# Performance work log

Hardware: AMD Instinct MI355X
Metric: run time of the kernel (lower is better)

## Reference

```python
import jax, jax.numpy as jnp
import numpy as np

BETA_MAX = 0.01
CD_WEIGHT = 1.0
FIDELITY_WEIGHT = 0.5
BETA = BETA_MAX  # fully annealed (step >= beta_warmup)
EPS = 1e-12


def _pairwise_dist(a, b):
    """Euclidean distance matrix. a: [B,N,3], b: [B,M,3] -> [B,N,M]."""
    a2 = jnp.sum(a * a, axis=-1)                      # [B,N]
    b2 = jnp.sum(b * b, axis=-1)                      # [B,M]
    ab = jnp.einsum('bnd,bmd->bnm', a, b)             # [B,N,M]
    sq = a2[:, :, None] + b2[:, None, :] - 2.0 * ab
    return jnp.sqrt(jnp.maximum(sq, EPS))


def chamfer_distance_l1(pred, full):
    d = _pairwise_dist(pred, full)                    # [B,N,M]
    d_pf = jnp.min(d, axis=2)                         # pred -> full, [B,N]
    d_fp = jnp.min(d, axis=1)                         # full -> pred, [B,M]
    return 0.5 * (jnp.mean(d_pf) + jnp.mean(d_fp))


def fidelity_loss(partial, pred):
    # one-directional: every partial point should have a close predicted point
    d = _pairwise_dist(partial, pred)                 # [B,P,N]
    return jnp.mean(jnp.min(d, axis=2))


def kl_divergence(mu, logvar):
    # -0.5 * E_batch[ sum_dim (1 + logvar - mu^2 - exp(logvar)) ]
    kl = -0.5 * jnp.sum(1.0 + logvar - mu * mu - jnp.exp(logvar), axis=1)
    return jnp.mean(kl)


def setup_inputs() -> dict:
    key = jax.random.key(0)
    k1, k2, k3, k4, k5 = jax.random.split(key, 5)
    B, N, P, D = 8, 8192, 2048, 512
    return {
        'pred': jax.random.normal(k1, (B, N, 3), dtype=jnp.float32),
        'full': jax.random.normal(k2, (B, N, 3), dtype=jnp.float32),
        'partial': jax.random.normal(k3, (B, P, 3), dtype=jnp.float32),
        'mu': jax.random.normal(k4, (B, D), dtype=jnp.float32),
        'logvar': jax.random.normal(k5, (B, D), dtype=jnp.float32) * 0.1,
    }


def reference(pred, full, partial, mu, logvar):
    cd = chamfer_distance_l1(pred, full)
    kl = kl_divergence(mu, logvar)
    fidel = fidelity_loss(partial, pred)
    total = CD_WEIGHT * cd + BETA * kl + FIDELITY_WEIGHT * fidel
    return (total, cd, kl, fidel)
```

## Files before the change

kernel.cpp:

```cpp
#include <hip/hip_runtime.h>
#include <math.h>

#define BATCH 8
#define NPTS  8192
#define PPTS  2048
#define DLAT  512

typedef __attribute__((ext_vector_type(8)))  short short8;
typedef __attribute__((ext_vector_type(16))) float floatx16;

#define SEG      (2 * BATCH * NPTS + BATCH * PPTS)
#define DIR_PF   0
#define DIR_FP   (BATCH * NPTS)
#define DIR_FID  (2 * BATCH * NPTS)
#define OFF_SEG  8

#define CHUNK  512
#define XBLK   512

__device__ __forceinline__ unsigned short f2bf(float f) {
    unsigned int u = __float_as_uint(f);
    return (unsigned short)((u + 0x7FFFu + ((u >> 16) & 1u)) >> 16);
}
__device__ __forceinline__ float bf2f(unsigned short s) {
    return __uint_as_float(((unsigned int)s) << 16);
}

__device__ __forceinline__ float min16(floatx16 d, float prev) {
    float a0 = fminf(fminf(d[0],  d[1]),  d[2]);
    float a1 = fminf(fminf(d[3],  d[4]),  d[5]);
    float a2 = fminf(fminf(d[6],  d[7]),  d[8]);
    float a3 = fminf(fminf(d[9],  d[10]), d[11]);
    float a4 = fminf(fminf(d[12], d[13]), d[14]);
    float b0 = fminf(fminf(a0, a1), a2);
    float b1 = fminf(fminf(a3, a4), d[15]);
    return fminf(fminf(b0, b1), prev);
}

__device__ __forceinline__ void encodeY(float y0, float y1, float y2,
                                        uint4* r0, uint4* r1) {
    const unsigned short h0 = f2bf(y0), h1 = f2bf(y1), h2 = f2bf(y2);
    const unsigned short l0 = f2bf(y0 - bf2f(h0));
    const unsigned short l1 = f2bf(y1 - bf2f(h1));
    const unsigned short l2 = f2bf(y2 - bf2f(h2));
    const float yn = fmaf(y0, y0, fmaf(y1, y1, y2 * y2));
    const unsigned short nh = f2bf(yn);
    const unsigned short nl = f2bf(yn - bf2f(nh));
    r0->x = (unsigned int)h0 | ((unsigned int)h1 << 16);
    r0->y = (unsigned int)h2 | ((unsigned int)l0 << 16);
    r0->z = (unsigned int)l1 | ((unsigned int)l2 << 16);
    r0->w = (unsigned int)h0 | ((unsigned int)h1 << 16);
    r1->x = (unsigned int)h2 | ((unsigned int)nh << 16);
    r1->y = (unsigned int)nl;
    r1->z = 0u; r1->w = 0u;
}

__global__ __launch_bounds__(256, 4) void minpass_kernel(
        const float* __restrict__ pred,
        const float* __restrict__ full,
        const float* __restrict__ partial,
        float* __restrict__ wsf,
        int ysplit) {
    const int bid = blockIdx.x;
    const int ys  = bid % ysplit;
    const int r   = bid / ysplit;
    const int b   = r / 36;
    const int s   = r % 36;
    const int yhalf = NPTS / ysplit;

    const int t = threadIdx.x;

    if (bid == 0) {
        if (t < 4) wsf[t] = 0.0f;
        if (t == 4) ((unsigned int*)wsf)[4] = 0u;
    }

    const float* xset; const float* yset; int minoff; int xbase;
    if (s < 16)      { xset = pred;    yset = full; xbase = b*NPTS + s*XBLK;
                       minoff = OFF_SEG + ys*SEG + DIR_PF  + b*NPTS + s*XBLK; }
    else if (s < 32) { xset = full;    yset = pred; xbase = b*NPTS + (s-16)*XBLK;
                       minoff = OFF_SEG + ys*SEG + DIR_FP  + b*NPTS + (s-16)*XBLK; }
    else             { xset = partial; yset = pred; xbase = b*PPTS + (s-32)*XBLK;
                       minoff = OFF_SEG + ys*SEG + DIR_FID + b*PPTS + (s-32)*XBLK; }

    const int lane = t & 63;
    const int wid  = t >> 6;
    const int l31  = lane & 31;
    const int half = lane >> 5;

    __shared__ uint4 sY[2][CHUNK];
    __shared__ uint4 sX[2][XBLK];
    __shared__ float sXn[XBLK];

    for (int i = t; i < XBLK; i += 256) {
        const float* xp = xset + (size_t)(xbase + i) * 3;
        const float x0 = xp[0], x1 = xp[1], x2 = xp[2];
        const float m0 = -2.0f*x0, m1 = -2.0f*x1, m2 = -2.0f*x2;
        const unsigned short h0 = f2bf(m0), h1 = f2bf(m1), h2 = f2bf(m2);
        const unsigned short l0 = f2bf(m0 - bf2f(h0));
        const unsigned short l1 = f2bf(m1 - bf2f(h1));
        const unsigned short l2 = f2bf(m2 - bf2f(h2));
        const unsigned int one = 0x3F80u;
        uint4 r0, r1;
        r0.x = (unsigned int)h0 | ((unsigned int)h1 << 16);
        r0.y = (unsigned int)h2 | ((unsigned int)h0 << 16);
        r0.z = (unsigned int)h1 | ((unsigned int)h2 << 16);
        r0.w = (unsigned int)l0 | ((unsigned int)l1 << 16);
        r1.x = (unsigned int)l2 | (one << 16);
        r1.y = one;
        r1.z = 0u; r1.w = 0u;
        sX[0][i] = r0; sX[1][i] = r1;
        sXn[i] = fmaf(x0, x0, fmaf(x1, x1, x2 * x2));
    }
    __syncthreads();

    const int xw = wid * 128;
    const short8 bf0 = *(const short8*)&sX[half][xw + l31];
    const short8 bf1 = *(const short8*)&sX[half][xw + 32 + l31];
    const short8 bf2 = *(const short8*)&sX[half][xw + 64 + l31];
    const short8 bf3 = *(const short8*)&sX[half][xw + 96 + l31];
    const float  xn0 = sXn[xw + l31];
    const float  xn1 = sXn[xw + 32 + l31];
    const float  xn2 = sXn[xw + 64 + l31];
    const float  xn3 = sXn[xw + 96 + l31];

    const floatx16 zc = {0,0,0,0, 0,0,0,0, 0,0,0,0, 0,0,0,0};
    float cmin0 = 3.4e38f, cmin1 = 3.4e38f, cmin2 = 3.4e38f, cmin3 = 3.4e38f;

    const float* ypts = yset + (size_t)(b * NPTS + ys * yhalf) * 3;

    for (int c = 0; c < yhalf; c += CHUNK) {
        __syncthreads();
        for (int i = t; i < CHUNK; i += 256) {
            const float* yp = ypts + (size_t)(c + i) * 3;
            uint4 r0, r1;
            encodeY(yp[0], yp[1], yp[2], &r0, &r1);
            sY[0][i] = r0; sY[1][i] = r1;
        }
        __syncthreads();

        const uint4* sYh = &sY[half][0];
        short8 af = *(const short8*)&sYh[l31];
#pragma unroll
        for (int j = 0; j < CHUNK / 32; ++j) {
            short8 afn = af;
            if (j + 1 < CHUNK / 32)
                afn = *(const short8*)&sYh[(j + 1) * 32 + l31];
            const floatx16 d0 = __builtin_amdgcn_mfma_f32_32x32x16_bf16(af, bf0, zc, 0, 0, 0);
            const floatx16 d1 = __builtin_amdgcn_mfma_f32_32x32x16_bf16(af, bf1, zc, 0, 0, 0);
            cmin0 = min16(d0, cmin0);
            const floatx16 d2 = __builtin_amdgcn_mfma_f32_32x32x16_bf16(af, bf2, zc, 0, 0, 0);
            cmin1 = min16(d1, cmin1);
            const floatx16 d3 = __builtin_amdgcn_mfma_f32_32x32x16_bf16(af, bf3, zc, 0, 0, 0);
            cmin2 = min16(d2, cmin2);
            cmin3 = min16(d3, cmin3);
            af = afn;
        }
    }

    const float m0 = fminf(cmin0, __shfl_xor(cmin0, 32, 64));
    const float m1 = fminf(cmin1, __shfl_xor(cmin1, 32, 64));
    const float m2 = fminf(cmin2, __shfl_xor(cmin2, 32, 64));
    const float m3 = fminf(cmin3, __shfl_xor(cmin3, 32, 64));
    if (lane < 32) {
        wsf[minoff + xw + l31]      = fmaxf(m0 + xn0, 0.0f);
        wsf[minoff + xw + 32 + l31] = fmaxf(m1 + xn1, 0.0f);
        wsf[minoff + xw + 64 + l31] = fmaxf(m2 + xn2, 0.0f);
        wsf[minoff + xw + 96 + l31] = fmaxf(m3 + xn3, 0.0f);
    }
}

__device__ __forceinline__ float waveReduceSum(float v) {
#pragma unroll
    for (int o = 32; o > 0; o >>= 1) v += __shfl_down(v, o, 64);
    return v;
}

__device__ __forceinline__ float blockReduceSum(float v) {
    __shared__ float wsum[4];
    const int lane = threadIdx.x & 63;
    const int wid  = threadIdx.x >> 6;
    v = waveReduceSum(v);
    if (lane == 0) wsum[wid] = v;
    __syncthreads();
    if (wid == 0) {
        v = (lane < ((int)blockDim.x >> 6)) ? wsum[lane] : 0.0f;
        v = waveReduceSum(v);
    }
    return v;
}

#define NRED_BLOCKS 145
__global__ __launch_bounds__(256) void reduce_finalize_kernel(
        float* __restrict__ wsf,
        const float* __restrict__ mu,
        const float* __restrict__ logvar,
        float* __restrict__ out,
        int ysplit) {
    float* acc = wsf;
    unsigned int* cnt = (unsigned int*)wsf + 4;
    const int bid = blockIdx.x;
    const int t   = threadIdx.x;

    float v = 0.0f;
    int accIdx;
    if (bid < 144) {
        int base;
        if (bid < 64)       { accIdx = 0; base = DIR_PF  + bid * 1024;         }
        else if (bid < 128) { accIdx = 1; base = DIR_FP  + (bid - 64) * 1024;  }
        else                { accIdx = 2; base = DIR_FID + (bid - 128) * 1024; }
#pragma unroll
        for (int k = 0; k < 4; ++k) {
            const int i = OFF_SEG + base + k * 256 + t;
            float m = wsf[i];
            for (int sg = 1; sg < ysplit; ++sg) m = fminf(m, wsf[sg * SEG + i]);
            v += sqrtf(fmaxf(m, 1e-12f));
        }
    } else {
        accIdx = 3;
#pragma unroll
        for (int k = 0; k < BATCH * DLAT / 256; ++k) {
            const int i = k * 256 + t;
            const float m = mu[i];
            const float l = logvar[i];
            v += -0.5f * (1.0f + l - m * m - expf(l));
        }
    }

    v = blockReduceSum(v);
    if (t == 0) {
        atomicAdd(&acc[accIdx], v);
        __threadfence();
        const unsigned int done = atomicAdd(cnt, 1u);
        if (done == NRED_BLOCKS - 1) {
            const float s_pf  = atomicAdd(&acc[0], 0.0f);
            const float s_fp  = atomicAdd(&acc[1], 0.0f);
            const float s_fid = atomicAdd(&acc[2], 0.0f);
            const float s_kl  = atomicAdd(&acc[3], 0.0f);
            const float cd  = 0.5f * (s_pf / (float)(BATCH * NPTS) +
                                      s_fp / (float)(BATCH * NPTS));
            const float fid = s_fid / (float)(BATCH * PPTS);
            const float kl  = s_kl / (float)BATCH;
            out[0] = cd + 0.01f * kl + 0.5f * fid;
            out[1] = cd;
            out[2] = kl;
            out[3] = fid;
        }
    }
}

extern "C" void kernel_launch(void* const* d_in, const int* in_sizes, int n_in,
                              void* d_out, int out_size, void* d_ws, size_t ws_size,
                              hipStream_t stream) {
    const float* pred    = (const float*)d_in[0];
    const float* full    = (const float*)d_in[1];
    const float* partial = (const float*)d_in[2];
    const float* mu      = (const float*)d_in[3];
    const float* logvar  = (const float*)d_in[4];
    float* out = (float*)d_out;
    float* wsf = (float*)d_ws;

    const size_t need4 = (size_t)(OFF_SEG + 4 * SEG) * 4;
    const int ysplit = (ws_size >= need4) ? 4 : 2;

    minpass_kernel<<<8 * 36 * ysplit, 256, 0, stream>>>(pred, full, partial, wsf, ysplit);

    reduce_finalize_kernel<<<NRED_BLOCKS, 256, 0, stream>>>(wsf, mu, logvar, out, ysplit);
}
```

Measured before the change: 104.7 us.

## Use v_min3 for min reduction, load X operands directly, widen reduce grid

The 16-way min reduction now uses inline v_min3_f32 instructions instead of chained fminf calls. Each lane builds its MFMA B-operand fragments and norms straight from global memory, which removes the shared-memory staging of X and one block barrier. The finalize kernel goes from 145 to 577 blocks, each reducing 256 elements instead of 1024, to raise parallelism. In exchange, the atomic-add contention on the accumulators and the completion counter rises, and each X point is encoded redundantly by both half-waves.

```diff
diff --git a/kernel.cpp b/kernel.cpp
--- a/kernel.cpp
+++ b/kernel.cpp
@@ -26,15 +26,21 @@
     return __uint_as_float(((unsigned int)s) << 16);
 }
 
+__device__ __forceinline__ float min3f(float a, float b, float c) {
+    float d;
+    asm("v_min3_f32 %0, %1, %2, %3" : "=v"(d) : "v"(a), "v"(b), "v"(c));
+    return d;
+}
+
 __device__ __forceinline__ float min16(floatx16 d, float prev) {
-    float a0 = fminf(fminf(d[0],  d[1]),  d[2]);
-    float a1 = fminf(fminf(d[3],  d[4]),  d[5]);
-    float a2 = fminf(fminf(d[6],  d[7]),  d[8]);
-    float a3 = fminf(fminf(d[9],  d[10]), d[11]);
-    float a4 = fminf(fminf(d[12], d[13]), d[14]);
-    float b0 = fminf(fminf(a0, a1), a2);
-    float b1 = fminf(fminf(a3, a4), d[15]);
-    return fminf(fminf(b0, b1), prev);
+    const float a0 = min3f(d[0],  d[1],  d[2]);
+    const float a1 = min3f(d[3],  d[4],  d[5]);
+    const float a2 = min3f(d[6],  d[7],  d[8]);
+    const float a3 = min3f(d[9],  d[10], d[11]);
+    const float a4 = min3f(d[12], d[13], d[14]);
+    const float b0 = min3f(a0, a1, a2);
+    const float b1 = min3f(a3, a4, d[15]);
+    return min3f(b0, b1, prev);
 }
 
 __device__ __forceinline__ void encodeY(float y0, float y1, float y2,
@@ -89,11 +95,13 @@
     const int half = lane >> 5;
 
     __shared__ uint4 sY[2][CHUNK];
-    __shared__ uint4 sX[2][XBLK];
-    __shared__ float sXn[XBLK];
-
-    for (int i = t; i < XBLK; i += 256) {
-        const float* xp = xset + (size_t)(xbase + i) * 3;
+
+    const int xw = wid * 128;
+    short8 bf0, bf1, bf2, bf3;
+    float  xn0, xn1, xn2, xn3;
+#pragma unroll
+    for (int k = 0; k < 4; ++k) {
+        const float* xp = xset + (size_t)(xbase + xw + k * 32 + l31) * 3;
         const float x0 = xp[0], x1 = xp[1], x2 = xp[2];
         const float m0 = -2.0f*x0, m1 = -2.0f*x1, m2 = -2.0f*x2;
         const unsigned short h0 = f2bf(m0), h1 = f2bf(m1), h2 = f2bf(m2);
@@ -109,20 +117,14 @@
         r1.x = (unsigned int)l2 | (one << 16);
         r1.y = one;
         r1.z = 0u; r1.w = 0u;
-        sX[0][i] = r0; sX[1][i] = r1;
-        sXn[i] = fmaf(x0, x0, fmaf(x1, x1, x2 * x2));
-    }
-    __syncthreads();
-
-    const int xw = wid * 128;
-    const short8 bf0 = *(const short8*)&sX[half][xw + l31];
-    const short8 bf1 = *(const short8*)&sX[half][xw + 32 + l31];
-    const short8 bf2 = *(const short8*)&sX[half][xw + 64 + l31];
-    const short8 bf3 = *(const short8*)&sX[half][xw + 96 + l31];
-    const float  xn0 = sXn[xw + l31];
-    const float  xn1 = sXn[xw + 32 + l31];
-    const float  xn2 = sXn[xw + 64 + l31];
-    const float  xn3 = sXn[xw + 96 + l31];
+        const uint4 rec = half ? r1 : r0;
+        const short8 bfv = *(const short8*)&rec;
+        const float  xnv = fmaf(x0, x0, fmaf(x1, x1, x2 * x2));
+        if (k == 0) { bf0 = bfv; xn0 = xnv; }
+        else if (k == 1) { bf1 = bfv; xn1 = xnv; }
+        else if (k == 2) { bf2 = bfv; xn2 = xnv; }
+        else { bf3 = bfv; xn3 = xnv; }
+    }
 
     const floatx16 zc = {0,0,0,0, 0,0,0,0, 0,0,0,0, 0,0,0,0};
     float cmin0 = 3.4e38f, cmin1 = 3.4e38f, cmin2 = 3.4e38f, cmin3 = 3.4e38f;
@@ -190,7 +192,7 @@
     return v;
 }
 
-#define NRED_BLOCKS 145
+#define NRED_BLOCKS 577
 __global__ __launch_bounds__(256) void reduce_finalize_kernel(
         float* __restrict__ wsf,
         const float* __restrict__ mu,
@@ -204,18 +206,15 @@
 
     float v = 0.0f;
     int accIdx;
-    if (bid < 144) {
+    if (bid < 576) {
         int base;
-        if (bid < 64)       { accIdx = 0; base = DIR_PF  + bid * 1024;         }
-        else if (bid < 128) { accIdx = 1; base = DIR_FP  + (bid - 64) * 1024;  }
-        else                { accIdx = 2; base = DIR_FID + (bid - 128) * 1024; }
-#pragma unroll
-        for (int k = 0; k < 4; ++k) {
-            const int i = OFF_SEG + base + k * 256 + t;
-            float m = wsf[i];
-            for (int sg = 1; sg < ysplit; ++sg) m = fminf(m, wsf[sg * SEG + i]);
-            v += sqrtf(fmaxf(m, 1e-12f));
-        }
+        if (bid < 256)      { accIdx = 0; base = DIR_PF  + bid * 256;         }
+        else if (bid < 512) { accIdx = 1; base = DIR_FP  + (bid - 256) * 256; }
+        else                { accIdx = 2; base = DIR_FID + (bid - 512) * 256; }
+        const int i = OFF_SEG + base + t;
+        float m = wsf[i];
+        for (int sg = 1; sg < ysplit; ++sg) m = fminf(m, wsf[sg * SEG + i]);
+        v = sqrtf(fmaxf(m, 1e-12f));
     } else {
         accIdx = 3;
 #pragma unroll
```

Measured after the change: 115.5 us. 10.3% more time.
